# Kernel tuning notes

Hardware: AMD Instinct MI355X
Metric: run time of the kernel (lower is better)

## Reference

```python
import jax, jax.numpy as jnp
import numpy as np

C = 256
NUM_HEADS = 8
GROUPS = C // 8
EPS = 1e-5


def conv1x1(x, w, b=None):
    # x: (B,C,H,W), w: (O,C)
    y = jnp.einsum('bchw,oc->bohw', x, w)
    if b is not None:
        y = y + b[None, :, None, None]
    return y


def dwconv3x3_s2(x, w):
    # depthwise 3x3, stride 2, padding 1; w: (C,1,3,3)
    return jax.lax.conv_general_dilated(
        x, w, window_strides=(2, 2), padding=((1, 1), (1, 1)),
        feature_group_count=x.shape[1],
        dimension_numbers=('NCHW', 'OIHW', 'NCHW'))


def group_norm(x, scale, bias, groups=GROUPS, eps=EPS):
    B, Cc, H, W = x.shape
    xg = x.reshape(B, groups, Cc // groups, H, W)
    mu = xg.mean(axis=(2, 3, 4), keepdims=True)
    var = xg.var(axis=(2, 3, 4), keepdims=True)
    xn = (xg - mu) * jax.lax.rsqrt(var + eps)
    return xn.reshape(B, Cc, H, W) * scale[None, :, None, None] + bias[None, :, None, None]


def silu(x):
    return x * jax.nn.sigmoid(x)


def downsample_branch(x, dw, gn1_s, gn1_b, pw, gn2_s, gn2_b):
    y = dwconv3x3_s2(x, dw)
    y = silu(group_norm(y, gn1_s, gn1_b))
    y = conv1x1(y, pw)
    y = silu(group_norm(y, gn2_s, gn2_b))
    return y


def setup_inputs() -> dict:
    key = jax.random.key(0)
    ks = jax.random.split(key, 20)
    s = 1.0 / np.sqrt(C)
    inp = {
        'x': jax.random.normal(ks[0], (32, C, 32, 32), dtype=jnp.float32),
        'wq': jax.random.normal(ks[1], (C, C), dtype=jnp.float32) * s,
        'bq': jnp.zeros((C,), jnp.float32),
        'wk': jax.random.normal(ks[2], (C, C), dtype=jnp.float32) * s,
        'bk': jnp.zeros((C,), jnp.float32),
        'wv': jax.random.normal(ks[3], (C, C), dtype=jnp.float32) * s,
        'bv': jnp.zeros((C,), jnp.float32),
        'k_dw': jax.random.normal(ks[4], (C, 1, 3, 3), dtype=jnp.float32) * (1.0 / 3.0),
        'k_gn1_s': jnp.ones((C,), jnp.float32), 'k_gn1_b': jnp.zeros((C,), jnp.float32),
        'k_pw': jax.random.normal(ks[5], (C, C), dtype=jnp.float32) * s,
        'k_gn2_s': jnp.ones((C,), jnp.float32), 'k_gn2_b': jnp.zeros((C,), jnp.float32),
        'v_dw': jax.random.normal(ks[6], (C, 1, 3, 3), dtype=jnp.float32) * (1.0 / 3.0),
        'v_gn1_s': jnp.ones((C,), jnp.float32), 'v_gn1_b': jnp.zeros((C,), jnp.float32),
        'v_pw': jax.random.normal(ks[7], (C, C), dtype=jnp.float32) * s,
        'v_gn2_s': jnp.ones((C,), jnp.float32), 'v_gn2_b': jnp.zeros((C,), jnp.float32),
    }
    return inp


def reference(x, wq, bq, wk, bk, wv, bv,
              k_dw, k_gn1_s, k_gn1_b, k_pw, k_gn2_s, k_gn2_b,
              v_dw, v_gn1_s, v_gn1_b, v_pw, v_gn2_s, v_gn2_b):
    B, Cc, H, W = x.shape
    nh = NUM_HEADS
    Dh = Cc // nh
    q = conv1x1(x, wq, bq)
    k = conv1x1(x, wk, bk)
    v = conv1x1(x, wv, bv)
    k = downsample_branch(k, k_dw, k_gn1_s, k_gn1_b, k_pw, k_gn2_s, k_gn2_b)
    v = downsample_branch(v, v_dw, v_gn1_s, v_gn1_b, v_pw, v_gn2_s, v_gn2_b)
    # view (B, nh, Dh, N) then transpose to (B, nh, N, Dh)
    qh = q.reshape(B, nh, Dh, -1).transpose(0, 1, 3, 2)
    kh = k.reshape(B, nh, Dh, -1).transpose(0, 1, 3, 2)
    vh = v.reshape(B, nh, Dh, -1).transpose(0, 1, 3, 2)
    scores = jnp.einsum('bhnd,bhmd->bhnm', qh, kh) / jnp.sqrt(jnp.float32(Dh))
    attn = jax.nn.softmax(scores, axis=-1)
    out = jnp.einsum('bhnm,bhmd->bhnd', attn, vh)  # (B,nh,N,Dh)
    out = out.transpose(0, 1, 3, 2).reshape(B, Cc, H, W)
    return out
```

## Files before the change

### kernel.cpp

```cpp
#include <hip/hip_runtime.h>
#include <cstddef>

#define B_  32
#define C_  256
#define N_  1024
#define M_  256
#define NH_ 8
#define DH_ 32

typedef __attribute__((ext_vector_type(4))) float f32x4;
typedef _Float16 half8h __attribute__((ext_vector_type(8)));
typedef _Float16 half4h __attribute__((ext_vector_type(4)));
typedef _Float16 half2h __attribute__((ext_vector_type(2)));

#define GLD16(g, l) __builtin_amdgcn_global_load_lds( \
    (const __attribute__((address_space(1))) unsigned int*)(g), \
    (__attribute__((address_space(3))) unsigned int*)(l), 16, 0, 0)

__global__ __launch_bounds__(256) void prep(
    const float* __restrict__ x,
    const float* __restrict__ w0, const float* __restrict__ w1,
    const float* __restrict__ w2, const float* __restrict__ w3,
    const float* __restrict__ w4,
    _Float16* __restrict__ xt, _Float16* __restrict__ wf5)
{
    const int bx = blockIdx.x;
    const int tid = threadIdx.x;

    if (bx < 2048) {
        __shared__ float tile[64][65];
        const int k0 = (bx & 3) * 64;
        const int n0 = ((bx >> 2) & 15) * 64;
        const int b  = bx >> 6;
        #pragma unroll
        for (int i = 0; i < 4; ++i) {
            const int kl = (tid >> 4) + i * 16;
            float4 v = *(const float4*)&x[((size_t)(b * C_) + k0 + kl) * N_ + n0 + (tid & 15) * 4];
            tile[(tid & 15) * 4 + 0][kl] = v.x;
            tile[(tid & 15) * 4 + 1][kl] = v.y;
            tile[(tid & 15) * 4 + 2][kl] = v.z;
            tile[(tid & 15) * 4 + 3][kl] = v.w;
        }
        __syncthreads();
        #pragma unroll
        for (int i = 0; i < 4; ++i) {
            const int nl = (tid >> 4) + i * 16;
            const int kl = (tid & 15) * 4;
            half4h hv;
            hv[0] = (_Float16)tile[nl][kl + 0];
            hv[1] = (_Float16)tile[nl][kl + 1];
            hv[2] = (_Float16)tile[nl][kl + 2];
            hv[3] = (_Float16)tile[nl][kl + 3];
            *(half4h*)&xt[((size_t)(b * N_) + n0 + nl) * C_ + k0 + kl] = hv;
        }
    } else {
        const int wb = bx - 2048;
        const int which = wb >> 4;
        const int off0  = (wb & 15) * 4096;
        const float* src = which == 0 ? w0 : which == 1 ? w1 : which == 2 ? w2
                          : which == 3 ? w3 : w4;
        _Float16* dst = wf5 + (size_t)which * 65536 + off0;
        #pragma unroll
        for (int j = 0; j < 16; ++j)
            dst[tid + j * 256] = (_Float16)src[off0 + tid + j * 256];
    }
}

__global__ __launch_bounds__(256) void qkv_gemm(
    const _Float16* __restrict__ wf5, const _Float16* __restrict__ XT,
    const float* __restrict__ bq, const float* __restrict__ bk,
    const float* __restrict__ bv,
    _Float16* __restrict__ yq, _Float16* __restrict__ yk,
    _Float16* __restrict__ yv)
{
    __shared__ _Float16 Ah[128][32];
    __shared__ _Float16 Bh[128][32];

    const int z = blockIdx.z;
    const int which = z >> 5;
    const int b = z & 31;
    const _Float16* Wf = wf5 + (size_t)which * 65536;
    const float* bias = which == 0 ? bq : which == 1 ? bk : bv;
    _Float16* Y = which == 0 ? yq : which == 1 ? yk : yv;

    const int row0 = blockIdx.x * 128;
    const int n0   = blockIdx.y * 128;
    const int tid  = threadIdx.x;
    const int lane = tid & 63, w = tid >> 6;
    const int wm = (w >> 1) * 64, wn = (w & 1) * 64;
    const int l16 = lane & 15, lq = lane >> 4;

    const _Float16* XTb = XT + ((size_t)(b * N_) + n0) * C_;

    const int sr = lane >> 2;
    const int sc = (lane & 3) * 8;
    const _Float16* Ag0 = Wf  + (size_t)(row0 + w * 32 + sr) * C_ + sc;
    const _Float16* Ag1 = Ag0 + (size_t)16 * C_;
    const _Float16* Bg0 = XTb + (size_t)(w * 32 + sr) * C_ + sc;
    const _Float16* Bg1 = Bg0 + (size_t)16 * C_;
    _Float16* ldsA0 = &Ah[w * 32][0];
    _Float16* ldsA1 = &Ah[w * 32 + 16][0];
    _Float16* ldsB0 = &Bh[w * 32][0];
    _Float16* ldsB1 = &Bh[w * 32 + 16][0];

    f32x4 acc[4][4];
    #pragma unroll
    for (int i = 0; i < 4; ++i)
        #pragma unroll
        for (int j = 0; j < 4; ++j)
            #pragma unroll
            for (int r = 0; r < 4; ++r) acc[i][j][r] = 0.f;

    for (int k0 = 0; k0 < C_; k0 += 32) {
        __syncthreads();
        GLD16(Ag0 + k0, ldsA0);
        GLD16(Ag1 + k0, ldsA1);
        GLD16(Bg0 + k0, ldsB0);
        GLD16(Bg1 + k0, ldsB1);
        __syncthreads();

        half8h af[4], bf[4];
        #pragma unroll
        for (int t = 0; t < 4; ++t) {
            af[t] = *(const half8h*)&Ah[wm + t * 16 + l16][lq * 8];
            bf[t] = *(const half8h*)&Bh[wn + t * 16 + l16][lq * 8];
        }
        #pragma unroll
        for (int mt = 0; mt < 4; ++mt)
            #pragma unroll
            for (int nt = 0; nt < 4; ++nt)
                acc[mt][nt] = __builtin_amdgcn_mfma_f32_16x16x32_f16(af[mt], bf[nt], acc[mt][nt], 0, 0, 0);
    }

    if (which == 0) {
        const float qs = 0.17677669529663687f * 1.4426950408889634f;
        #pragma unroll
        for (int mt = 0; mt < 4; ++mt) {
            const int row = row0 + wm + mt * 16 + lq * 4;
            const float4 bv4 = *(const float4*)&bias[row];
            const int h  = row >> 5;
            const int d0 = row & 31;
            _Float16* yh = Y + ((size_t)(b * NH_) + h) * N_ * DH_ + d0;
            #pragma unroll
            for (int nt = 0; nt < 4; ++nt) {
                const int n = n0 + wn + nt * 16 + l16;
                half4h hv;
                hv[0] = (_Float16)((acc[mt][nt][0] + bv4.x) * qs);
                hv[1] = (_Float16)((acc[mt][nt][1] + bv4.y) * qs);
                hv[2] = (_Float16)((acc[mt][nt][2] + bv4.z) * qs);
                hv[3] = (_Float16)((acc[mt][nt][3] + bv4.w) * qs);
                *(half4h*)&yh[(size_t)n * DH_] = hv;
            }
        }
    } else {
        #pragma unroll
        for (int mt = 0; mt < 4; ++mt) {
            #pragma unroll
            for (int r = 0; r < 4; ++r) {
                const int row = row0 + wm + mt * 16 + lq * 4 + r;
                const float bv_ = bias[row];
                #pragma unroll
                for (int nt = 0; nt < 4; ++nt)
                    Y[((size_t)(b * C_) + row) * N_ + n0 + wn + nt * 16 + l16] =
                        (_Float16)(acc[mt][nt][r] + bv_);
            }
        }
    }
}

__global__ __launch_bounds__(256) void dw_gn(
    const _Float16* __restrict__ kin, const _Float16* __restrict__ vin,
    const float* __restrict__ kdw, const float* __restrict__ vdw,
    const float* __restrict__ kg1s, const float* __restrict__ kg1b,
    const float* __restrict__ vg1s, const float* __restrict__ vg1b,
    _Float16* __restrict__ kdT, _Float16* __restrict__ vdT)
{
    __shared__ _Float16 Xs[8192];
    __shared__ float red[8];
    const int bx = blockIdx.x;
    const int branch = bx >> 10;
    const int b = (bx >> 5) & 31;
    const int g = bx & 31;
    const _Float16* in = branch ? vin : kin;
    const float* dw = branch ? vdw : kdw;
    const float* gs = branch ? vg1s : kg1s;
    const float* gb = branch ? vg1b : kg1b;
    _Float16* outT = branch ? vdT : kdT;

    const int tid = threadIdx.x;

    {
        const _Float16* src = in + ((size_t)(b * C_) + g * 8) * 1024;
        #pragma unroll
        for (int i = 0; i < 4; ++i)
            *(half8h*)&Xs[tid * 8 + i * 2048] =
                *(const half8h*)&src[tid * 8 + i * 2048];
    }
    __syncthreads();

    const int oy = tid >> 4, ox = tid & 15;
    const int iy0 = oy*2 - 1, ix0 = ox*2 - 1;

    float vals[8];
    float s1 = 0.f, s2 = 0.f;
    #pragma unroll
    for (int cc = 0; cc < 8; ++cc) {
        const int c = g*8 + cc;
        const _Float16* ip = &Xs[cc * 1024];
        const float* wp = dw + c*9;
        float s = 0.f;
        #pragma unroll
        for (int dy = 0; dy < 3; ++dy) {
            const int iy = iy0 + dy;
            if (iy < 0 || iy > 31) continue;
            #pragma unroll
            for (int dx = 0; dx < 3; ++dx) {
                const int ix = ix0 + dx;
                if (ix < 0 || ix > 31) continue;
                s += (float)ip[iy*32 + ix] * wp[dy*3 + dx];
            }
        }
        vals[cc] = s;
        s1 += s; s2 += s*s;
    }
    #pragma unroll
    for (int off = 32; off > 0; off >>= 1) {
        s1 += __shfl_down(s1, off);
        s2 += __shfl_down(s2, off);
    }
    const int lane = tid & 63, wid = tid >> 6;
    if (lane == 0) { red[wid] = s1; red[4 + wid] = s2; }
    __syncthreads();
    s1 = red[0] + red[1] + red[2] + red[3];
    s2 = red[4] + red[5] + red[6] + red[7];
    const float mean = s1 * (1.f/2048.f);
    const float var  = s2 * (1.f/2048.f) - mean*mean;
    const float rstd = rsqrtf(var + 1e-5f);

    half8h o;
    #pragma unroll
    for (int cc = 0; cc < 8; ++cc) {
        const int c = g*8 + cc;
        const float xn = (vals[cc] - mean) * rstd * gs[c] + gb[c];
        o[cc] = (_Float16)(xn / (1.f + __expf(-xn)));
    }
    *(half8h*)&outT[((size_t)(b * M_) + tid) * C_ + g * 8] = o;
}

__global__ __launch_bounds__(256) void pw_gn2(
    const _Float16* __restrict__ wf5,
    const _Float16* __restrict__ kdT, const _Float16* __restrict__ vdT,
    const float* __restrict__ kg2s, const float* __restrict__ kg2b,
    const float* __restrict__ vg2s, const float* __restrict__ vg2b,
    _Float16* __restrict__ k2, _Float16* __restrict__ v2)
{
    __shared__ _Float16 Wlds[32][264];
    __shared__ _Float16 Bs[256][32];
    __shared__ float gmean[4], grstd[4];

    const int ch0 = blockIdx.x * 32;
    const int b   = blockIdx.y;
    const int branch = blockIdx.z;
    const _Float16* Wsrc = wf5 + (size_t)(3 + branch) * 65536;
    const _Float16* inT = branch ? vdT : kdT;
    const float* gs = branch ? vg2s : kg2s;
    const float* gb = branch ? vg2b : kg2b;
    _Float16* outp = branch ? v2 : k2;

    const int tid = threadIdx.x;
    const int lane = tid & 63, w = tid >> 6;
    const int l16 = lane & 15, quad = lane >> 4;

    {
        const int row = tid >> 3;
        const int off = (tid & 7) * 32;
        #pragma unroll
        for (int j = 0; j < 4; ++j)
            *(int4*)&Wlds[row][off + j * 8] =
                *(const int4*)&Wsrc[(size_t)(ch0 + row) * C_ + off + j * 8];
    }

    f32x4 acc[2][4];
    #pragma unroll
    for (int i = 0; i < 2; ++i)
        #pragma unroll
        for (int j = 0; j < 4; ++j)
            #pragma unroll
            for (int r = 0; r < 4; ++r) acc[i][j][r] = 0.f;

    const _Float16* inb = inT + (size_t)(b * M_) * C_;
    const int sr = lane >> 2;
    const int sc = (lane & 3) * 8;
    const _Float16* Bg = inb + (size_t)(w * 64 + sr) * C_ + sc;

    for (int k0 = 0; k0 < C_; k0 += 32) {
        __syncthreads();
        GLD16(Bg + k0,             &Bs[w * 64][0]);
        GLD16(Bg + 16 * C_ + k0,   &Bs[w * 64 + 16][0]);
        GLD16(Bg + 32 * C_ + k0,   &Bs[w * 64 + 32][0]);
        GLD16(Bg + 48 * C_ + k0,   &Bs[w * 64 + 48][0]);
        __syncthreads();

        half8h af[2], bf[4];
        #pragma unroll
        for (int mt = 0; mt < 2; ++mt)
            af[mt] = *(const half8h*)&Wlds[mt * 16 + l16][k0 + quad * 8];
        #pragma unroll
        for (int nt = 0; nt < 4; ++nt)
            bf[nt] = *(const half8h*)&Bs[w * 64 + nt * 16 + l16][quad * 8];
        #pragma unroll
        for (int mt = 0; mt < 2; ++mt)
            #pragma unroll
            for (int nt = 0; nt < 4; ++nt)
                acc[mt][nt] = __builtin_amdgcn_mfma_f32_16x16x32_f16(af[mt], bf[nt], acc[mt][nt], 0, 0, 0);
    }

    __syncthreads();
    _Float16 (*Rs)[264] = Wlds;
    #pragma unroll
    for (int mt = 0; mt < 2; ++mt)
        #pragma unroll
        for (int nt = 0; nt < 4; ++nt)
            #pragma unroll
            for (int r = 0; r < 4; ++r)
                Rs[mt * 16 + quad * 4 + r][w * 64 + nt * 16 + l16] = (_Float16)acc[mt][nt][r];
    __syncthreads();

    {
        float s1 = 0.f, s2 = 0.f;
        #pragma unroll
        for (int r = 0; r < 8; ++r)
            #pragma unroll
            for (int j = 0; j < 4; ++j) {
                const float vv = (float)Rs[w * 8 + r][lane * 4 + j];
                s1 += vv; s2 += vv * vv;
            }
        #pragma unroll
        for (int off = 32; off > 0; off >>= 1) {
            s1 += __shfl_xor(s1, off);
            s2 += __shfl_xor(s2, off);
        }
        if (lane == 0) {
            const float mean = s1 * (1.f / 2048.f);
            const float var  = s2 * (1.f / 2048.f) - mean * mean;
            gmean[w] = mean;
            grstd[w] = rsqrtf(var + 1e-5f);
        }
    }
    __syncthreads();

    #pragma unroll
    for (int cc = 0; cc < 32; ++cc) {
        const int g = cc >> 3;
        const float xn = ((float)Rs[cc][tid] - gmean[g]) * grstd[g] * gs[ch0 + cc] + gb[ch0 + cc];
        const float y  = xn / (1.f + __expf(-xn));
        outp[((size_t)(b * C_) + ch0 + cc) * M_ + tid] = (_Float16)y;
    }
}

__global__ __launch_bounds__(512) void attention_mfma(
    const _Float16* __restrict__ qT, const _Float16* __restrict__ k,
    const _Float16* __restrict__ v, float* __restrict__ out)
{
    __shared__ _Float16 Kl[256][40];
    __shared__ _Float16 VT[32][264];

    const int bh = blockIdx.y;
    const int b = bh >> 3, h = bh & 7;
    const int n0 = blockIdx.x * 256;
    const int tid = threadIdx.x;
    const int lane = tid & 63, w = tid >> 6;
    const int l16 = lane & 15, quad = lane >> 4;
    const float SHIFT = 8.0f * 1.4426950408889634f;
    const f32x4 initS = {-SHIFT, -SHIFT, -SHIFT, -SHIFT};

    const size_t kvbase = ((size_t)(b * C_) + h * DH_) * (size_t)M_;

    {
        const int d2 = (tid & 15) * 2;
        const int m0 = (tid >> 4) * 8;
        half8h ka = *(const half8h*)&k[kvbase + (size_t)d2 * M_ + m0];
        half8h kb = *(const half8h*)&k[kvbase + (size_t)(d2 + 1) * M_ + m0];
        #pragma unroll
        for (int j = 0; j < 8; ++j) {
            union { _Float16 h[2]; unsigned u; } pk;
            pk.h[0] = ka[j]; pk.h[1] = kb[j];
            *(unsigned*)&Kl[m0 + j][d2] = pk.u;
        }
        const int vd  = tid & 31;
        const int vm0 = (tid >> 5) * 16;
        #pragma unroll
        for (int i = 0; i < 2; ++i)
            *(half8h*)&VT[vd][vm0 + i * 8] =
                *(const half8h*)&v[kvbase + (size_t)vd * M_ + vm0 + i * 8];
    }

    const int qn = n0 + w * 32 + l16;
    const _Float16* qbase = qT + (((size_t)(b * NH_) + h) * N_ + qn) * DH_ + quad * 8;
    half8h qf[2];
    qf[0] = *(const half8h*)&qbase[0];
    qf[1] = *(const half8h*)&qbase[16 * DH_];

    __syncthreads();

    f32x4 O[2][2];
    #pragma unroll
    for (int qt = 0; qt < 2; ++qt)
        #pragma unroll
        for (int dt = 0; dt < 2; ++dt)
            #pragma unroll
            for (int r = 0; r < 4; ++r) O[qt][dt][r] = 0.f;
    float lsum[2] = {0.f, 0.f};

    #pragma unroll
    for (int ch = 0; ch < 2; ++ch) {
        f32x4 S[2][8];
        __builtin_amdgcn_s_setprio(1);
        #pragma unroll
        for (int kt = 0; kt < 8; ++kt) {
            half8h kf = *(const half8h*)&Kl[ch * 128 + kt * 16 + l16][quad * 8];
            S[0][kt] = __builtin_amdgcn_mfma_f32_16x16x32_f16(kf, qf[0], initS, 0, 0, 0);
            S[1][kt] = __builtin_amdgcn_mfma_f32_16x16x32_f16(kf, qf[1], initS, 0, 0, 0);
        }
        __builtin_amdgcn_s_setprio(0);
        #pragma unroll
        for (int qt = 0; qt < 2; ++qt)
            #pragma unroll
            for (int kt = 0; kt < 8; ++kt)
                #pragma unroll
                for (int r = 0; r < 4; ++r) {
                    const float p = exp2f(S[qt][kt][r]);
                    S[qt][kt][r] = p;
                    lsum[qt] += p;
                }
        __builtin_amdgcn_s_setprio(1);
        #pragma unroll
        for (int kt = 0; kt < 8; ++kt) {
            half4h vf[2];
            #pragma unroll
            for (int dt = 0; dt < 2; ++dt)
                vf[dt] = *(const half4h*)&VT[dt * 16 + l16][ch * 128 + kt * 16 + quad * 4];
            #pragma unroll
            for (int qt = 0; qt < 2; ++qt) {
                half2h p01 = __builtin_bit_cast(half2h,
                    __builtin_amdgcn_cvt_pkrtz(S[qt][kt][0], S[qt][kt][1]));
                half2h p23 = __builtin_bit_cast(half2h,
                    __builtin_amdgcn_cvt_pkrtz(S[qt][kt][2], S[qt][kt][3]));
                half4h pf = __builtin_shufflevector(p01, p23, 0, 1, 2, 3);
                #pragma unroll
                for (int dt = 0; dt < 2; ++dt)
                    O[qt][dt] = __builtin_amdgcn_mfma_f32_16x16x16f16(vf[dt], pf, O[qt][dt], 0, 0, 0);
            }
        }
        __builtin_amdgcn_s_setprio(0);
    }

    #pragma unroll
    for (int qt = 0; qt < 2; ++qt) {
        float ls = lsum[qt];
        ls += __shfl_xor(ls, 16);
        ls += __shfl_xor(ls, 32);
        const float inv = 1.f / ls;
        #pragma unroll
        for (int dt = 0; dt < 2; ++dt)
            #pragma unroll
            for (int r = 0; r < 4; ++r) {
                const int drow = h * DH_ + dt * 16 + quad * 4 + r;
                out[((size_t)(b * C_) + drow) * N_ + qn + qt * 16] = O[qt][dt][r] * inv;
            }
    }
}

extern "C" void kernel_launch(void* const* d_in, const int* in_sizes, int n_in,
                              void* d_out, int out_size, void* d_ws, size_t ws_size,
                              hipStream_t stream)
{
    const float* x    = (const float*)d_in[0];
    const float* wq   = (const float*)d_in[1];
    const float* bq   = (const float*)d_in[2];
    const float* wk   = (const float*)d_in[3];
    const float* bk   = (const float*)d_in[4];
    const float* wv   = (const float*)d_in[5];
    const float* bv   = (const float*)d_in[6];
    const float* kdw  = (const float*)d_in[7];
    const float* kg1s = (const float*)d_in[8];
    const float* kg1b = (const float*)d_in[9];
    const float* kpw  = (const float*)d_in[10];
    const float* kg2s = (const float*)d_in[11];
    const float* kg2b = (const float*)d_in[12];
    const float* vdw  = (const float*)d_in[13];
    const float* vg1s = (const float*)d_in[14];
    const float* vg1b = (const float*)d_in[15];
    const float* vpw  = (const float*)d_in[16];
    const float* vg2s = (const float*)d_in[17];
    const float* vg2b = (const float*)d_in[18];
    float* out = (float*)d_out;

    const size_t HCN = (size_t)B_ * C_ * N_;
    const size_t HCM = (size_t)B_ * C_ * M_;
    _Float16* qh  = (_Float16*)d_ws;
    _Float16* k0h = qh  + HCN;
    _Float16* v0h = k0h + HCN;
    _Float16* XT  = v0h + HCN;
    _Float16* Wf5 = XT  + HCN;
    _Float16* kdT = Wf5 + 5 * 65536;
    _Float16* vdT = kdT + HCM;
    _Float16* k2  = vdT + HCM;
    _Float16* v2  = k2  + HCM;

    dim3 blk(256);

    prep<<<dim3(2128), blk, 0, stream>>>(x, wq, wk, wv, kpw, vpw, XT, Wf5);
    qkv_gemm<<<dim3(2, 8, 96), blk, 0, stream>>>(Wf5, XT, bq, bk, bv, qh, k0h, v0h);
    dw_gn<<<dim3(2048), blk, 0, stream>>>(k0h, v0h, kdw, vdw,
                                          kg1s, kg1b, vg1s, vg1b, kdT, vdT);
    pw_gn2<<<dim3(8, 32, 2), blk, 0, stream>>>(Wf5, kdT, vdT,
                                               kg2s, kg2b, vg2s, vg2b, k2, v2);
    attention_mfma<<<dim3(4, B_ * NH_), dim3(512), 0, stream>>>(qh, k2, v2, out);
}
```

Before: 199.4 us.

## Widen GEMM K-tiles to 64 with XOR-swizzled LDS and XCD-aware block remap

Both the QKV projection GEMM and the pointwise GEMM now stage 64-wide K slices instead of 32. This halves the number of barrier pairs per K loop. An XOR swizzle on the LDS column index spreads the fragment reads across banks to reduce conflicts. The 3D grids are flattened into 1D and remapped so that consecutive blocks landing on the same XCD (flat & 7) share batch and weight data for better L2 locality. LDS use per block doubles for the staging buffers, which may lower occupancy.

```diff
diff --git a/kernel.cpp b/kernel.cpp
--- a/kernel.cpp
+++ b/kernel.cpp
@@ -73,18 +73,23 @@
     _Float16* __restrict__ yq, _Float16* __restrict__ yk,
     _Float16* __restrict__ yv)
 {
-    __shared__ _Float16 Ah[128][32];
-    __shared__ _Float16 Bh[128][32];
-
-    const int z = blockIdx.z;
-    const int which = z >> 5;
-    const int b = z & 31;
+    __shared__ _Float16 Ah[128][64];
+    __shared__ _Float16 Bh[128][64];
+
+    const int flat    = blockIdx.x;
+    const int logical = (flat & 7) * 192 + (flat >> 3);
+    const int b       = logical / 48;
+    const int r48     = logical % 48;
+    const int which   = r48 >> 4;
+    const int x       = r48 & 1;
+    const int y       = (r48 >> 1) & 7;
+
     const _Float16* Wf = wf5 + (size_t)which * 65536;
     const float* bias = which == 0 ? bq : which == 1 ? bk : bv;
     _Float16* Y = which == 0 ? yq : which == 1 ? yk : yv;
 
-    const int row0 = blockIdx.x * 128;
-    const int n0   = blockIdx.y * 128;
+    const int row0 = x * 128;
+    const int n0   = y * 128;
     const int tid  = threadIdx.x;
     const int lane = tid & 63, w = tid >> 6;
     const int wm = (w >> 1) * 64, wn = (w & 1) * 64;
@@ -92,16 +97,10 @@
 
     const _Float16* XTb = XT + ((size_t)(b * N_) + n0) * C_;
 
-    const int sr = lane >> 2;
-    const int sc = (lane & 3) * 8;
-    const _Float16* Ag0 = Wf  + (size_t)(row0 + w * 32 + sr) * C_ + sc;
-    const _Float16* Ag1 = Ag0 + (size_t)16 * C_;
-    const _Float16* Bg0 = XTb + (size_t)(w * 32 + sr) * C_ + sc;
-    const _Float16* Bg1 = Bg0 + (size_t)16 * C_;
-    _Float16* ldsA0 = &Ah[w * 32][0];
-    _Float16* ldsA1 = &Ah[w * 32 + 16][0];
-    _Float16* ldsB0 = &Bh[w * 32][0];
-    _Float16* ldsB1 = &Bh[w * 32 + 16][0];
+    const int sr8 = lane >> 3;
+    const int scs = ((lane & 7) ^ sr8) * 8;
+    const _Float16* Ag = Wf  + (size_t)(row0 + w * 32 + sr8) * C_ + scs;
+    const _Float16* Bg = XTb + (size_t)(w * 32 + sr8) * C_ + scs;
 
     f32x4 acc[4][4];
     #pragma unroll
@@ -111,25 +110,31 @@
             #pragma unroll
             for (int r = 0; r < 4; ++r) acc[i][j][r] = 0.f;
 
-    for (int k0 = 0; k0 < C_; k0 += 32) {
+    for (int k0 = 0; k0 < C_; k0 += 64) {
         __syncthreads();
-        GLD16(Ag0 + k0, ldsA0);
-        GLD16(Ag1 + k0, ldsA1);
-        GLD16(Bg0 + k0, ldsB0);
-        GLD16(Bg1 + k0, ldsB1);
+        #pragma unroll
+        for (int g = 0; g < 4; ++g) {
+            GLD16(Ag + (size_t)(g * 8) * C_ + k0, &Ah[w * 32 + g * 8][0]);
+            GLD16(Bg + (size_t)(g * 8) * C_ + k0, &Bh[w * 32 + g * 8][0]);
+        }
         __syncthreads();
 
-        half8h af[4], bf[4];
-        #pragma unroll
-        for (int t = 0; t < 4; ++t) {
-            af[t] = *(const half8h*)&Ah[wm + t * 16 + l16][lq * 8];
-            bf[t] = *(const half8h*)&Bh[wn + t * 16 + l16][lq * 8];
-        }
-        #pragma unroll
-        for (int mt = 0; mt < 4; ++mt)
-            #pragma unroll
-            for (int nt = 0; nt < 4; ++nt)
-                acc[mt][nt] = __builtin_amdgcn_mfma_f32_16x16x32_f16(af[mt], bf[nt], acc[mt][nt], 0, 0, 0);
+        #pragma unroll
+        for (int kk = 0; kk < 2; ++kk) {
+            half8h af[4], bf[4];
+            #pragma unroll
+            for (int t = 0; t < 4; ++t) {
+                const int ra = wm + t * 16 + l16;
+                af[t] = *(const half8h*)&Ah[ra][(((kk << 2) | lq) ^ (ra & 7)) * 8];
+                const int rb = wn + t * 16 + l16;
+                bf[t] = *(const half8h*)&Bh[rb][(((kk << 2) | lq) ^ (rb & 7)) * 8];
+            }
+            #pragma unroll
+            for (int mt = 0; mt < 4; ++mt)
+                #pragma unroll
+                for (int nt = 0; nt < 4; ++nt)
+                    acc[mt][nt] = __builtin_amdgcn_mfma_f32_16x16x32_f16(af[mt], bf[nt], acc[mt][nt], 0, 0, 0);
+        }
     }
 
     if (which == 0) {
@@ -255,12 +260,16 @@
     _Float16* __restrict__ k2, _Float16* __restrict__ v2)
 {
     __shared__ _Float16 Wlds[32][264];
-    __shared__ _Float16 Bs[256][32];
+    __shared__ _Float16 Bs[256][64];
     __shared__ float gmean[4], grstd[4];
 
-    const int ch0 = blockIdx.x * 32;
-    const int b   = blockIdx.y;
-    const int branch = blockIdx.z;
+    const int flat    = blockIdx.x;
+    const int logical = (flat & 7) * 64 + (flat >> 3);
+    const int xx      = logical & 7;
+    const int b       = (logical >> 3) & 31;
+    const int branch  = logical >> 8;
+
+    const int ch0 = xx * 32;
     const _Float16* Wsrc = wf5 + (size_t)(3 + branch) * 65536;
     const _Float16* inT = branch ? vdT : kdT;
     const float* gs = branch ? vg2s : kg2s;
@@ -289,30 +298,34 @@
             for (int r = 0; r < 4; ++r) acc[i][j][r] = 0.f;
 
     const _Float16* inb = inT + (size_t)(b * M_) * C_;
-    const int sr = lane >> 2;
-    const int sc = (lane & 3) * 8;
-    const _Float16* Bg = inb + (size_t)(w * 64 + sr) * C_ + sc;
-
-    for (int k0 = 0; k0 < C_; k0 += 32) {
+    const int sr8 = lane >> 3;
+    const int scs = ((lane & 7) ^ sr8) * 8;
+    const _Float16* Bg = inb + (size_t)(w * 64 + sr8) * C_ + scs;
+
+    for (int k0 = 0; k0 < C_; k0 += 64) {
         __syncthreads();
-        GLD16(Bg + k0,             &Bs[w * 64][0]);
-        GLD16(Bg + 16 * C_ + k0,   &Bs[w * 64 + 16][0]);
-        GLD16(Bg + 32 * C_ + k0,   &Bs[w * 64 + 32][0]);
-        GLD16(Bg + 48 * C_ + k0,   &Bs[w * 64 + 48][0]);
+        #pragma unroll
+        for (int g = 0; g < 8; ++g)
+            GLD16(Bg + (size_t)(g * 8) * C_ + k0, &Bs[w * 64 + g * 8][0]);
         __syncthreads();
 
-        half8h af[2], bf[4];
-        #pragma unroll
-        for (int mt = 0; mt < 2; ++mt)
-            af[mt] = *(const half8h*)&Wlds[mt * 16 + l16][k0 + quad * 8];
-        #pragma unroll
-        for (int nt = 0; nt < 4; ++nt)
-            bf[nt] = *(const half8h*)&Bs[w * 64 + nt * 16 + l16][quad * 8];
-        #pragma unroll
-        for (int mt = 0; mt < 2; ++mt)
-            #pragma unroll
-            for (int nt = 0; nt < 4; ++nt)
-                acc[mt][nt] = __builtin_amdgcn_mfma_f32_16x16x32_f16(af[mt], bf[nt], acc[mt][nt], 0, 0, 0);
+        #pragma unroll
+        for (int kk = 0; kk < 2; ++kk) {
+            half8h af[2], bf[4];
+            #pragma unroll
+            for (int mt = 0; mt < 2; ++mt)
+                af[mt] = *(const half8h*)&Wlds[mt * 16 + l16][k0 + kk * 32 + quad * 8];
+            #pragma unroll
+            for (int nt = 0; nt < 4; ++nt) {
+                const int rb = w * 64 + nt * 16 + l16;
+                bf[nt] = *(const half8h*)&Bs[rb][(((kk << 2) | quad) ^ (rb & 7)) * 8];
+            }
+            #pragma unroll
+            for (int mt = 0; mt < 2; ++mt)
+                #pragma unroll
+                for (int nt = 0; nt < 4; ++nt)
+                    acc[mt][nt] = __builtin_amdgcn_mfma_f32_16x16x32_f16(af[mt], bf[nt], acc[mt][nt], 0, 0, 0);
+        }
     }
 
     __syncthreads();
@@ -511,10 +524,10 @@
     dim3 blk(256);
 
     prep<<<dim3(2128), blk, 0, stream>>>(x, wq, wk, wv, kpw, vpw, XT, Wf5);
-    qkv_gemm<<<dim3(2, 8, 96), blk, 0, stream>>>(Wf5, XT, bq, bk, bv, qh, k0h, v0h);
+    qkv_gemm<<<dim3(1536), blk, 0, stream>>>(Wf5, XT, bq, bk, bv, qh, k0h, v0h);
     dw_gn<<<dim3(2048), blk, 0, stream>>>(k0h, v0h, kdw, vdw,
                                           kg1s, kg1b, vg1s, vg1b, kdT, vdT);
-    pw_gn2<<<dim3(8, 32, 2), blk, 0, stream>>>(Wf5, kdT, vdT,
-                                               kg2s, kg2b, vg2s, vg2b, k2, v2);
+    pw_gn2<<<dim3(512), blk, 0, stream>>>(Wf5, kdT, vdT,
+                                          kg2s, kg2b, vg2s, vg2b, k2, v2);
     attention_mfma<<<dim3(4, B_ * NH_), dim3(512), 0, stream>>>(qh, k2, v2, out);
 }
```

Measured after the change: 186.6 us. 1.07x faster.
